# Performance work log

Hardware: AMD Instinct MI355X
Metric: run time of the kernel (lower is better)

The kernel has to match this reference:

```python
import jax, jax.numpy as jnp
import numpy as np

SCALE = 100.0
ALPHA_MEM = 0.9
ALPHA_P = 0.99
ALPHA_MEM_OUT = 0.9

@jax.custom_vjp
def spike(x):
    return (x > 0).astype(x.dtype)

def _spike_fwd(x):
    return spike(x), x

def _spike_bwd(x, g):
    return (g / (SCALE * jnp.abs(x) + 1.0) ** 2,)

spike.defvjp(_spike_fwd, _spike_bwd)

B, T, N_IN, N, N_OUT = 64, 200, 128, 2048, 20

def setup_inputs() -> dict:
    key = jax.random.key(0)
    ks = jax.random.split(key, 6)
    inputs = jax.random.normal(ks[0], (B, T, N_IN), dtype=jnp.float32)
    w = jax.random.normal(ks[1], (N, N), dtype=jnp.float32) / np.sqrt(N)
    wscale_in = 1.0 - ALPHA_MEM
    w_in = jax.random.normal(ks[2], (N_IN, N), dtype=jnp.float32) * (wscale_in / np.sqrt(N_IN))
    wscale_out = 1.0 - ALPHA_MEM_OUT
    w_out = jax.random.normal(ks[3], (N, N_OUT), dtype=jnp.float32) * (wscale_out / np.sqrt(N))
    w_signs = jnp.sign(jax.random.normal(ks[4], (N,), dtype=jnp.float32))
    p = 0.1 * jax.random.normal(ks[5], (N,), dtype=jnp.float32)
    return {"inputs": inputs, "w": w, "w_in": w_in, "w_out": w_out,
            "w_signs": w_signs, "p": p}

def reference(inputs, w, w_in, w_out, w_signs, p):
    dt = inputs.dtype
    h1 = jnp.einsum('btc,cn->btn', inputs, w_in)          # [B,T,N]
    rec_w = w_signs[:, None] * jnp.abs(w)                  # [N,N]
    depr = (p < 0).astype(dt)                              # [N]

    def step(carry, h1_t):
        mem, w_p = carry
        mthr = mem - 1.0
        out = spike(mthr)
        rst = jax.lax.stop_gradient((mthr > 0).astype(dt))
        syn_p = jnp.einsum('bn,no->bo', out * (1.0 + w_p), rec_w)
        w_p_new = w_p * ALPHA_P + out * p * (1.0 + depr * w_p)
        mem_new = ALPHA_MEM * mem + h1_t + syn_p - rst
        return (mem_new, w_p_new), out

    zeros = jnp.zeros((h1.shape[0], rec_w.shape[0]), dtype=dt)
    _, spk = jax.lax.scan(step, (zeros, zeros), jnp.swapaxes(h1, 0, 1))
    spk_rec = jnp.swapaxes(spk, 0, 1)                      # [B,T,N]

    h2 = jnp.einsum('btn,no->bto', spk_rec, w_out)         # [B,T,O]

    def out_step(o, h2_t):
        o2 = ALPHA_MEM_OUT * o + h2_t
        return o2, o2

    o0 = jnp.zeros((h2.shape[0], h2.shape[2]), dtype=dt)
    _, outs = jax.lax.scan(out_step, o0, jnp.swapaxes(h2, 0, 1))
    return jnp.swapaxes(outs, 0, 1)                        # [B,T,O]
```

## Files before the change

### kernel.cpp

```cpp
#include <hip/hip_runtime.h>

#define BB   64
#define TT   200
#define NIN  128
#define NN   2048
#define NOUT 20

#define S    8
#define NWIN 25
#define ACAP 64
#define BCAP 128

typedef __attribute__((ext_vector_type(8))) short short8;
typedef __attribute__((ext_vector_type(4))) float f32x4;

__device__ __forceinline__ void bf16split(float x, ushort& h, ushort& l) {
    unsigned u = __float_as_uint(x);
    unsigned hb = (u + 0x7FFFu + ((u >> 16) & 1u)) >> 16;
    h = (ushort)hb;
    float xh = __uint_as_float(hb << 16);
    float xl = x - xh;
    unsigned v = __float_as_uint(xl);
    l = (ushort)((v + 0x7FFFu + ((v >> 16) & 1u)) >> 16);
}

__global__ __launch_bounds__(256) void repack_a(
    const float* __restrict__ X, ushort* __restrict__ Ap)
{
    const int blk  = blockIdx.x;
    const int tid  = threadIdx.x;
    const int kc   = tid >> 6;
    const int lane = tid & 63;
    const int lr   = lane & 15, lg = lane >> 4;

    const float* src = X + (size_t)(blk * 16 + lr) * NIN + kc * 32 + lg * 8;
    float f[8];
    *(float4*)(f)     = *(const float4*)(src);
    *(float4*)(f + 4) = *(const float4*)(src + 4);

    short8 hv, lv;
    #pragma unroll
    for (int j = 0; j < 8; ++j) {
        ushort h, l;
        bf16split(f[j], h, l);
        hv[j] = (short)h; lv[j] = (short)l;
    }
    ushort* dst = Ap + (size_t)(blk * 4 + kc) * 1024 + lane * 8;
    *(short8*)(dst)       = hv;
    *(short8*)(dst + 512) = lv;
}

__global__ __launch_bounds__(256) void repack_b(
    const float* __restrict__ W, ushort* __restrict__ Bp)
{
    const int blk  = blockIdx.x;
    const int tid  = threadIdx.x;
    const int kc   = tid >> 6;
    const int lane = tid & 63;
    const int lr   = lane & 15, lg = lane >> 4;

    const float* src = W + (size_t)(kc * 32 + lg * 8) * NN + blk * 16 + lr;
    float f[8];
    #pragma unroll
    for (int j = 0; j < 8; ++j) f[j] = src[(size_t)j * NN];

    short8 hv, lv;
    #pragma unroll
    for (int j = 0; j < 8; ++j) {
        ushort h, l;
        bf16split(f[j], h, l);
        hv[j] = (short)h; lv[j] = (short)l;
    }
    ushort* dst = Bp + (size_t)(blk * 4 + kc) * 1024 + lane * 8;
    *(short8*)(dst)       = hv;
    *(short8*)(dst + 512) = lv;
}

__global__ __launch_bounds__(256, 2) void h1_mfma(
    const ushort* __restrict__ Ap, const ushort* __restrict__ Bp,
    float* __restrict__ C)
{
    const int l   = blockIdx.y * gridDim.x + blockIdx.x;
    const int nl  = (l & 7) * 200 + (l >> 3);
    const int bx  = nl & 15, by = nl >> 4;

    const int tid  = threadIdx.x;
    const int w_   = tid >> 6, lane = tid & 63;
    const int lr   = lane & 15, lg = lane >> 4;
    const int m0   = by * 128, n0 = bx * 128;
    const int wr   = (w_ >> 1) * 64, wc = (w_ & 1) * 64;

    const ushort* pA = Ap + (size_t)((m0 + wr) >> 4) * 4096 + lane * 8;
    const ushort* pB = Bp + (size_t)((n0 + wc) >> 4) * 4096 + lane * 8;

#define LDF(p) (*(const short8*)(p))
    short8 ah[2][4], al[2][4], bh[2][4], bl[2][4];
    #pragma unroll
    for (int rb = 0; rb < 4; ++rb) {
        ah[0][rb] = LDF(pA + rb * 4096);
        al[0][rb] = LDF(pA + rb * 4096 + 512);
        bh[0][rb] = LDF(pB + rb * 4096);
        bl[0][rb] = LDF(pB + rb * 4096 + 512);
    }

    f32x4 acc[4][4];
    const f32x4 z = {0.f, 0.f, 0.f, 0.f};
    #pragma unroll
    for (int rb = 0; rb < 4; ++rb)
        #pragma unroll
        for (int cb = 0; cb < 4; ++cb) acc[rb][cb] = z;

    #pragma unroll
    for (int kc = 0; kc < 4; ++kc) {
        const int cur = kc & 1, nxt = cur ^ 1;
        if (kc < 3) {
            const int ko = (kc + 1) * 1024;
            #pragma unroll
            for (int rb = 0; rb < 4; ++rb) {
                ah[nxt][rb] = LDF(pA + rb * 4096 + ko);
                al[nxt][rb] = LDF(pA + rb * 4096 + ko + 512);
                bh[nxt][rb] = LDF(pB + rb * 4096 + ko);
                bl[nxt][rb] = LDF(pB + rb * 4096 + ko + 512);
            }
        }
        #pragma unroll
        for (int rb = 0; rb < 4; ++rb)
            #pragma unroll
            for (int cb = 0; cb < 4; ++cb) {
                acc[rb][cb] = __builtin_amdgcn_mfma_f32_16x16x32_bf16(
                    bh[cur][cb], ah[cur][rb], acc[rb][cb], 0, 0, 0);
                acc[rb][cb] = __builtin_amdgcn_mfma_f32_16x16x32_bf16(
                    bl[cur][cb], ah[cur][rb], acc[rb][cb], 0, 0, 0);
                acc[rb][cb] = __builtin_amdgcn_mfma_f32_16x16x32_bf16(
                    bh[cur][cb], al[cur][rb], acc[rb][cb], 0, 0, 0);
            }
    }
#undef LDF

    #pragma unroll
    for (int rb = 0; rb < 4; ++rb) {
        float* Crow = C + (size_t)(m0 + wr + rb * 16 + lr) * NN + n0 + wc + lg * 4;
        #pragma unroll
        for (int cb = 0; cb < 4; ++cb)
            *(f32x4*)(Crow + cb * 16) = acc[rb][cb];
    }
}

__global__ __launch_bounds__(512) void snn_scan(
    const float* __restrict__ h1, const float* __restrict__ w,
    const float* __restrict__ w_signs, const float* __restrict__ pvec,
    const float* __restrict__ w_out, float* __restrict__ out)
{
    const int b   = blockIdx.x;
    const int tid = threadIdx.x;
    const int n0  = tid << 2;

    __shared__ int   s_amask[2];
    __shared__ int   s_acnt[2][S];
    __shared__ int   s_aidx[2][S][ACAP];
    __shared__ float s_aval[2][S][ACAP];
    __shared__ int   s_bcnt[2];
    __shared__ int   s_bidx[2][BCAP];
    __shared__ float s_bval[2][BCAP];

    if (tid < 2) { s_amask[tid] = 0; s_bcnt[tid] = 0; }
    if (tid < 2 * S) ((int*)s_acnt)[tid] = 0;

    float4 mem = {0.f,0.f,0.f,0.f}, wp = {0.f,0.f,0.f,0.f};
    const float4 p4 = *(const float4*)(pvec + n0);
    const float4 sg = *(const float4*)(w_signs + n0);
    float4 depr;
    depr.x = (p4.x < 0.f) ? 1.f : 0.f;  depr.y = (p4.y < 0.f) ? 1.f : 0.f;
    depr.z = (p4.z < 0.f) ? 1.f : 0.f;  depr.w = (p4.w < 0.f) ? 1.f : 0.f;

    const float P99[S] = {1.0f, 0.99f, 0.9801f, 0.970299f, 0.96059601f,
                          0.9509900499f, 0.941480149401f, 0.93206534790699f};
    const float P99_8 = 0.9227446944279201f;

    const float* hb = h1 + (size_t)b * TT * NN + n0;
    float* outb = out + (size_t)b * TT * NOUT + tid;
    float o2 = 0.f;

    float4 PA[S], PB[S];
    #pragma unroll
    for (int j = 0; j < S; ++j) PA[j] = *(const float4*)(hb + (size_t)j * NN);
    __syncthreads();

#define RAWBAR()                                              \
    do { asm volatile("s_waitcnt lgkmcnt(0)" ::: "memory");   \
         __builtin_amdgcn_s_barrier();                        \
         asm volatile("" ::: "memory"); } while (0)

    auto window = [&](float4 (&Pc)[S], float4 (&Pf)[S], int wnd) {
        const int p  = wnd & 1;
        const int t0 = wnd * S;
        const float4 memB = mem, wpB = wp;

        #pragma unroll
        for (int j = 0; j < S; ++j) {
            const float4 a = Pc[j];
            int tp = t0 + j + S; if (tp > TT - 1) tp = TT - 1;
            Pf[j] = *(const float4*)(hb + (size_t)tp * NN);

            const float mx = fmaxf(fmaxf(mem.x, mem.y), fmaxf(mem.z, mem.w));
            if (__builtin_expect(mx > 1.f, 0)) {
                const bool f0 = mem.x > 1.f, f1 = mem.y > 1.f,
                           f2 = mem.z > 1.f, f3 = mem.w > 1.f;
                atomicOr(&s_amask[p], 1 << j);
                if (f0) { int k = atomicAdd(&s_acnt[p][j], 1);
                          if (k < ACAP) { s_aidx[p][j][k] = n0;
                                          s_aval[p][j][k] = (1.f + wp.x * P99[j]) * sg.x; } }
                if (f1) { int k = atomicAdd(&s_acnt[p][j], 1);
                          if (k < ACAP) { s_aidx[p][j][k] = n0 + 1;
                                          s_aval[p][j][k] = (1.f + wp.y * P99[j]) * sg.y; } }
                if (f2) { int k = atomicAdd(&s_acnt[p][j], 1);
                          if (k < ACAP) { s_aidx[p][j][k] = n0 + 2;
                                          s_aval[p][j][k] = (1.f + wp.z * P99[j]) * sg.z; } }
                if (f3) { int k = atomicAdd(&s_acnt[p][j], 1);
                          if (k < ACAP) { s_aidx[p][j][k] = n0 + 3;
                                          s_aval[p][j][k] = (1.f + wp.w * P99[j]) * sg.w; } }
                mem.x = fmaf(0.9f, mem.x, a.x) - (f0 ? 1.f : 0.f);
                mem.y = fmaf(0.9f, mem.y, a.y) - (f1 ? 1.f : 0.f);
                mem.z = fmaf(0.9f, mem.z, a.z) - (f2 ? 1.f : 0.f);
                mem.w = fmaf(0.9f, mem.w, a.w) - (f3 ? 1.f : 0.f);
            } else {
                mem.x = fmaf(0.9f, mem.x, a.x);
                mem.y = fmaf(0.9f, mem.y, a.y);
                mem.z = fmaf(0.9f, mem.z, a.z);
                mem.w = fmaf(0.9f, mem.w, a.w);
            }
        }

        RAWBAR();
        const int mask = s_amask[p];

        if (__builtin_expect(mask == 0, 1)) {
            wp.x *= P99_8; wp.y *= P99_8; wp.z *= P99_8; wp.w *= P99_8;
            if (tid < NOUT) {
                #pragma unroll
                for (int j = 0; j < S; ++j) {
                    o2 = 0.9f * o2;
                    outb[(size_t)(t0 + j) * NOUT] = o2;
                }
            }
            return;
        }

        const int tstar = __ffs(mask) - 1;
        mem = memB; wp = wpB;
        #pragma unroll
        for (int j = 0; j < S; ++j) {
            const float4 a = Pc[j];
            if (j < tstar) {
                mem.x = fmaf(0.9f, mem.x, a.x);
                mem.y = fmaf(0.9f, mem.y, a.y);
                mem.z = fmaf(0.9f, mem.z, a.z);
                mem.w = fmaf(0.9f, mem.w, a.w);
                wp.x *= 0.99f; wp.y *= 0.99f; wp.z *= 0.99f; wp.w *= 0.99f;
                if (tid < NOUT) { o2 = 0.9f * o2;
                                  outb[(size_t)(t0 + j) * NOUT] = o2; }
            } else if (j == tstar) {
                const bool f0 = mem.x > 1.f, f1 = mem.y > 1.f,
                           f2 = mem.z > 1.f, f3 = mem.w > 1.f;
                int cnt = s_acnt[p][j]; if (cnt > ACAP) cnt = ACAP;
                float4 syn = {0.f,0.f,0.f,0.f};
                for (int m = 0; m < cnt; ++m) {
                    const int nm = s_aidx[p][j][m];
                    const float vm = s_aval[p][j][m];
                    const float4 wr = *(const float4*)(w + (size_t)nm * NN + n0);
                    syn.x = fmaf(vm, fabsf(wr.x), syn.x);
                    syn.y = fmaf(vm, fabsf(wr.y), syn.y);
                    syn.z = fmaf(vm, fabsf(wr.z), syn.z);
                    syn.w = fmaf(vm, fabsf(wr.w), syn.w);
                }
                if (tid < NOUT) {
                    float c = 0.f;
                    for (int m = 0; m < cnt; ++m)
                        c += w_out[(size_t)s_aidx[p][j][m] * NOUT + tid];
                    o2 = 0.9f * o2 + c;
                    outb[(size_t)(t0 + j) * NOUT] = o2;
                }
                mem.x = fmaf(0.9f, mem.x, a.x) + syn.x - (f0 ? 1.f : 0.f);
                mem.y = fmaf(0.9f, mem.y, a.y) + syn.y - (f1 ? 1.f : 0.f);
                mem.z = fmaf(0.9f, mem.z, a.z) + syn.z - (f2 ? 1.f : 0.f);
                mem.w = fmaf(0.9f, mem.w, a.w) + syn.w - (f3 ? 1.f : 0.f);
                wp.x = f0 ? 0.99f*wp.x + p4.x*(1.f + depr.x*wp.x) : 0.99f*wp.x;
                wp.y = f1 ? 0.99f*wp.y + p4.y*(1.f + depr.y*wp.y) : 0.99f*wp.y;
                wp.z = f2 ? 0.99f*wp.z + p4.z*(1.f + depr.z*wp.z) : 0.99f*wp.z;
                wp.w = f3 ? 0.99f*wp.w + p4.w*(1.f + depr.w*wp.w) : 0.99f*wp.w;
            } else {
                const int par = j & 1;
                const bool f0 = mem.x > 1.f, f1 = mem.y > 1.f,
                           f2 = mem.z > 1.f, f3 = mem.w > 1.f;
                if (f0 | f1 | f2 | f3) {
                    if (f0) { int k = atomicAdd(&s_bcnt[par], 1); if (k < BCAP) {
                              s_bidx[par][k] = n0;     s_bval[par][k] = (1.f + wp.x) * sg.x; } }
                    if (f1) { int k = atomicAdd(&s_bcnt[par], 1); if (k < BCAP) {
                              s_bidx[par][k] = n0 + 1; s_bval[par][k] = (1.f + wp.y) * sg.y; } }
                    if (f2) { int k = atomicAdd(&s_bcnt[par], 1); if (k < BCAP) {
                              s_bidx[par][k] = n0 + 2; s_bval[par][k] = (1.f + wp.z) * sg.z; } }
                    if (f3) { int k = atomicAdd(&s_bcnt[par], 1); if (k < BCAP) {
                              s_bidx[par][k] = n0 + 3; s_bval[par][k] = (1.f + wp.w) * sg.w; } }
                }
                RAWBAR();
                int cnt = s_bcnt[par]; if (cnt > BCAP) cnt = BCAP;
                float4 syn = {0.f,0.f,0.f,0.f};
                for (int m = 0; m < cnt; ++m) {
                    const int nm = s_bidx[par][m];
                    const float vm = s_bval[par][m];
                    const float4 wr = *(const float4*)(w + (size_t)nm * NN + n0);
                    syn.x = fmaf(vm, fabsf(wr.x), syn.x);
                    syn.y = fmaf(vm, fabsf(wr.y), syn.y);
                    syn.z = fmaf(vm, fabsf(wr.z), syn.z);
                    syn.w = fmaf(vm, fabsf(wr.w), syn.w);
                }
                if (tid < NOUT) {
                    float c = 0.f;
                    for (int m = 0; m < cnt; ++m)
                        c += w_out[(size_t)s_bidx[par][m] * NOUT + tid];
                    o2 = 0.9f * o2 + c;
                    outb[(size_t)(t0 + j) * NOUT] = o2;
                }
                mem.x = fmaf(0.9f, mem.x, a.x) + syn.x - (f0 ? 1.f : 0.f);
                mem.y = fmaf(0.9f, mem.y, a.y) + syn.y - (f1 ? 1.f : 0.f);
                mem.z = fmaf(0.9f, mem.z, a.z) + syn.z - (f2 ? 1.f : 0.f);
                mem.w = fmaf(0.9f, mem.w, a.w) + syn.w - (f3 ? 1.f : 0.f);
                wp.x = f0 ? 0.99f*wp.x + p4.x*(1.f + depr.x*wp.x) : 0.99f*wp.x;
                wp.y = f1 ? 0.99f*wp.y + p4.y*(1.f + depr.y*wp.y) : 0.99f*wp.y;
                wp.z = f2 ? 0.99f*wp.z + p4.z*(1.f + depr.z*wp.z) : 0.99f*wp.z;
                wp.w = f3 ? 0.99f*wp.w + p4.w*(1.f + depr.w*wp.w) : 0.99f*wp.w;
                RAWBAR();
                if (tid == 0) s_bcnt[par] = 0;
            }
        }
        RAWBAR();
        if (tid < S) s_acnt[p][tid] = 0;
        else if (tid == S) s_amask[p] = 0;
    };

    for (int wnd = 0; wnd < NWIN - 1; wnd += 2) {
        window(PA, PB, wnd);
        window(PB, PA, wnd + 1);
    }
    window(PA, PB, NWIN - 1);
#undef RAWBAR
}

extern "C" void kernel_launch(void* const* d_in, const int* in_sizes, int n_in,
                              void* d_out, int out_size, void* d_ws, size_t ws_size,
                              hipStream_t stream) {
    (void)in_sizes; (void)n_in; (void)out_size; (void)ws_size;
    const float* inputs  = (const float*)d_in[0];
    const float* w       = (const float*)d_in[1];
    const float* w_in    = (const float*)d_in[2];
    const float* w_out   = (const float*)d_in[3];
    const float* w_signs = (const float*)d_in[4];
    const float* p       = (const float*)d_in[5];
    float* out = (float*)d_out;

    const size_t H1B = (size_t)BB * TT * NN * 4;
    const size_t APB = (size_t)800 * 4096 * 2;

    float*  h1 = (float*)d_ws;
    ushort* Ap = (ushort*)((char*)d_ws + H1B);
    ushort* Bp = (ushort*)((char*)d_ws + H1B + APB);

    repack_a<<<800, 256, 0, stream>>>(inputs, Ap);
    repack_b<<<128, 256, 0, stream>>>(w_in, Bp);

    dim3 gg(NN / 128, (BB * TT) / 128);
    h1_mfma<<<gg, 256, 0, stream>>>(Ap, Bp, h1);

    snn_scan<<<BB, 512, 0, stream>>>(h1, w, w_signs, p, w_out, out);
}
```

Baseline: 97.12 us.

## Stage h1 GEMM operand tiles through LDS with async global_load_lds double buffering

The h1 MFMA GEMM kernel now loads its pre-packed bf16 hi/lo A and B tiles into double-buffered shared memory with direct global-to-LDS loads, then reads fragments from LDS. Before, each wave loaded its own fragments from global memory into registers, so tiles shared by several waves were fetched more than once. The change removes that duplicated global traffic and register double-buffering. In exchange it adds 64KB of LDS per block and block-wide barriers each k-step, which may reduce occupancy. The h1 GEMM is likely a small part of the total time next to the sequential scan kernel.

```diff
diff --git a/kernel.cpp b/kernel.cpp
--- a/kernel.cpp
+++ b/kernel.cpp
@@ -80,6 +80,8 @@
     const ushort* __restrict__ Ap, const ushort* __restrict__ Bp,
     float* __restrict__ C)
 {
+    __shared__ ushort sbuf[2][16][1024];
+
     const int l   = blockIdx.y * gridDim.x + blockIdx.x;
     const int nl  = (l & 7) * 200 + (l >> 3);
     const int bx  = nl & 15, by = nl >> 4;
@@ -90,18 +92,25 @@
     const int m0   = by * 128, n0 = bx * 128;
     const int wr   = (w_ >> 1) * 64, wc = (w_ & 1) * 64;
 
-    const ushort* pA = Ap + (size_t)((m0 + wr) >> 4) * 4096 + lane * 8;
-    const ushort* pB = Bp + (size_t)((n0 + wc) >> 4) * 4096 + lane * 8;
-
-#define LDF(p) (*(const short8*)(p))
-    short8 ah[2][4], al[2][4], bh[2][4], bl[2][4];
-    #pragma unroll
-    for (int rb = 0; rb < 4; ++rb) {
-        ah[0][rb] = LDF(pA + rb * 4096);
-        al[0][rb] = LDF(pA + rb * 4096 + 512);
-        bh[0][rb] = LDF(pB + rb * 4096);
-        bl[0][rb] = LDF(pB + rb * 4096 + 512);
-    }
+    const ushort* pAs = Ap + (size_t)(m0 >> 4) * 4096;
+    const ushort* pBs = Bp + (size_t)(n0 >> 4) * 4096;
+
+#define STAGE(kc, nb)                                                        \
+    do {                                                                     \
+        _Pragma("unroll")                                                    \
+        for (int i_ = 0; i_ < 8; ++i_) {                                     \
+            const int idx_   = w_ * 8 + i_;                                  \
+            const int side_  = idx_ >> 4;                                    \
+            const int chunk_ = (idx_ >> 1) & 7;                              \
+            const int hl_    = idx_ & 1;                                     \
+            const ushort* g_ = (side_ ? pBs : pAs) + chunk_ * 4096           \
+                               + (kc) * 1024 + hl_ * 512 + lane * 8;         \
+            ushort* d_ = &sbuf[nb][idx_ >> 1][hl_ * 512];                    \
+            __builtin_amdgcn_global_load_lds(                                \
+                (const __attribute__((address_space(1))) void*)g_,           \
+                (__attribute__((address_space(3))) void*)d_, 16, 0, 0);      \
+        }                                                                    \
+    } while (0)
 
     f32x4 acc[4][4];
     const f32x4 z = {0.f, 0.f, 0.f, 0.f};
@@ -110,32 +119,42 @@
         #pragma unroll
         for (int cb = 0; cb < 4; ++cb) acc[rb][cb] = z;
 
+    STAGE(0, 0);
+    __syncthreads();
+
+    const int ar = wr >> 4;
+    const int br = 8 + (wc >> 4);
+
     #pragma unroll
     for (int kc = 0; kc < 4; ++kc) {
-        const int cur = kc & 1, nxt = cur ^ 1;
-        if (kc < 3) {
-            const int ko = (kc + 1) * 1024;
-            #pragma unroll
-            for (int rb = 0; rb < 4; ++rb) {
-                ah[nxt][rb] = LDF(pA + rb * 4096 + ko);
-                al[nxt][rb] = LDF(pA + rb * 4096 + ko + 512);
-                bh[nxt][rb] = LDF(pB + rb * 4096 + ko);
-                bl[nxt][rb] = LDF(pB + rb * 4096 + ko + 512);
-            }
+        const int cb_ = kc & 1;
+        if (kc < 3) STAGE(kc + 1, cb_ ^ 1);
+
+        short8 fah[4], fal[4], fbh[4], fbl[4];
+        #pragma unroll
+        for (int rb = 0; rb < 4; ++rb) {
+            fah[rb] = *(const short8*)(&sbuf[cb_][ar + rb][lane * 8]);
+            fal[rb] = *(const short8*)(&sbuf[cb_][ar + rb][512 + lane * 8]);
+        }
+        #pragma unroll
+        for (int cb = 0; cb < 4; ++cb) {
+            fbh[cb] = *(const short8*)(&sbuf[cb_][br + cb][lane * 8]);
+            fbl[cb] = *(const short8*)(&sbuf[cb_][br + cb][512 + lane * 8]);
         }
         #pragma unroll
         for (int rb = 0; rb < 4; ++rb)
             #pragma unroll
             for (int cb = 0; cb < 4; ++cb) {
                 acc[rb][cb] = __builtin_amdgcn_mfma_f32_16x16x32_bf16(
-                    bh[cur][cb], ah[cur][rb], acc[rb][cb], 0, 0, 0);
+                    fbh[cb], fah[rb], acc[rb][cb], 0, 0, 0);
                 acc[rb][cb] = __builtin_amdgcn_mfma_f32_16x16x32_bf16(
-                    bl[cur][cb], ah[cur][rb], acc[rb][cb], 0, 0, 0);
+                    fbl[cb], fah[rb], acc[rb][cb], 0, 0, 0);
                 acc[rb][cb] = __builtin_amdgcn_mfma_f32_16x16x32_bf16(
-                    bh[cur][cb], al[cur][rb], acc[rb][cb], 0, 0, 0);
+                    fbh[cb], fal[rb], acc[rb][cb], 0, 0, 0);
             }
-    }
-#undef LDF
+        if (kc < 3) __syncthreads();
+    }
+#undef STAGE
 
     #pragma unroll
     for (int rb = 0; rb < 4; ++rb) {
```

Result: faster. 89.86 us (-7.5%).
